# Kernel tuning notes

Measured on AMD Instinct MI355X. Metric: run time of the kernel, lower is better.

The kernel has to match this reference:

```python
import jax, jax.numpy as jnp
import numpy as np

B, S, T, D = 8, 8, 256, 256          # batch, series, time_steps, input_dim
H, DK = 8, 64                         # attn_heads, attn_dim
HD = H * DK                           # 512
L = 2                                 # attn_layers
F = 256                               # mlp_dim
R = 512                               # resolution
M = 128                               # number of mid-points sampled this step
EPS = 1e-5


def setup_inputs() -> dict:
    key = jax.random.key(0)
    ks = iter(jax.random.split(key, 64))

    def rn(shape, scale=0.05):
        return scale * jax.random.normal(next(ks), shape, dtype=jnp.float32)

    inp = {
        'encoded': jax.random.normal(next(ks), (B, S, T, D), dtype=jnp.float32),
        'true_u': jax.random.uniform(next(ks), (B, S, T), dtype=jnp.float32),
        'mid_idx': jnp.sort(jax.random.randint(next(ks), (M,), 0, T)),
        'left_idx': jax.random.randint(next(ks), (M,), 0, T),
        'right_idx': jax.random.randint(next(ks), (M,), 0, T),
        'i': 3,
        # dimension_shift
        'ds_W': rn((D, HD)), 'ds_b': jnp.zeros((HD,), jnp.float32),
        # per-layer, per-head key-creator MLPs (stacked): (D+1) -> F -> F -> DK
        'kW1': rn((L, H, D + 1, F)), 'kb1': jnp.zeros((L, H, F), jnp.float32),
        'kW2': rn((L, H, F, F)),     'kb2': jnp.zeros((L, H, F), jnp.float32),
        'kW3': rn((L, H, F, DK)),    'kb3': jnp.zeros((L, H, DK), jnp.float32),
        # value-creator MLPs
        'vW1': rn((L, H, D + 1, F)), 'vb1': jnp.zeros((L, H, F), jnp.float32),
        'vW2': rn((L, H, F, F)),     'vb2': jnp.zeros((L, H, F), jnp.float32),
        'vW3': rn((L, H, F, DK)),    'vb3': jnp.zeros((L, H, DK), jnp.float32),
        # attention / feed-forward layer norms
        'ln1_g': jnp.ones((L, HD), jnp.float32), 'ln1_b': jnp.zeros((L, HD), jnp.float32),
        'ln2_g': jnp.ones((L, HD), jnp.float32), 'ln2_b': jnp.zeros((L, HD), jnp.float32),
        # feed-forwards
        'ffW1': rn((L, HD, HD)), 'ffb1': jnp.zeros((L, HD), jnp.float32),
        'ffW2': rn((L, HD, HD)), 'ffb2': jnp.zeros((L, HD), jnp.float32),
        # dist_extractors MLP: HD -> F -> F -> R
        'deW1': rn((HD, F)), 'deb1': jnp.zeros((F,), jnp.float32),
        'deW2': rn((F, F)),  'deb2': jnp.zeros((F,), jnp.float32),
        'deW3': rn((F, R)),  'deb3': jnp.zeros((R,), jnp.float32),
    }
    return inp


def _mlp_heads(x, W1, b1, W2, b2, W3, b3):
    # x: [B,S,T,D+1]; weights: [L,H,...] -> out [L,B,S,T,H,DK]
    h = jax.nn.relu(jnp.einsum('bstc,lhcf->lbsthf', x, W1) + b1[:, None, None, None])
    h = jax.nn.relu(jnp.einsum('lbsthf,lhfg->lbsthg', h, W2) + b2[:, None, None, None])
    return jnp.einsum('lbsthg,lhgd->lbsthd', h, W3) + b3[:, None, None, None]


def _ln(x, g, b):
    mu = jnp.mean(x, axis=-1, keepdims=True)
    var = jnp.mean(jnp.square(x - mu), axis=-1, keepdims=True)
    return (x - mu) * jax.lax.rsqrt(var + EPS) * g + b


def reference(encoded, true_u, mid_idx, left_idx, right_idx, i,
              ds_W, ds_b,
              kW1, kb1, kW2, kb2, kW3, kb3,
              vW1, vb1, vW2, vb2, vW3, vb3,
              ln1_g, ln1_b, ln2_g, ln2_b,
              ffW1, ffb1, ffW2, ffb2,
              deW1, deb1, deW2, deb2, deW3, deb3):
    # merged_input = cat([encoded, true_u[..., None]])  -> [B,S,T,D+1]
    merged = jnp.concatenate([encoded, true_u[..., None]], axis=-1)

    keys = _mlp_heads(merged, kW1, kb1, kW2, kb2, kW3, kb3)   # [L,B,S,T,H,DK]
    values = _mlp_heads(merged, vW1, vb1, vW2, vb2, vW3, vb3)  # [L,B,S,T,H,DK]

    srange = jnp.arange(S)
    # n=1 neighbor: time index = loop counter m for series < i, else right[m]
    # (faithful to keys_hist[:, :i, mid:mid+1] in the original)
    idx1 = jnp.where(srange[None, :] < i, jnp.arange(M)[:, None], right_idx[:, None])  # [M,S]

    def gather_neighbors(kv):  # kv: [L,B,S,T,H,DK] -> [L,B,M,S,2,H,DK]
        n0 = jnp.transpose(kv[:, :, :, left_idx], (0, 1, 3, 2, 4, 5))  # [L,B,M,S,H,DK]
        n1 = kv[:, :, srange[None, :], idx1]                            # [L,B,M,S,H,DK]
        return jnp.stack([n0, n1], axis=4)

    nk = gather_neighbors(keys)
    nv = gather_neighbors(values)

    pred = encoded[:, i, mid_idx]                  # [B,M,D]
    att_value = pred @ ds_W + ds_b                 # [B,M,HD]

    scale = DK ** (-0.5)
    for l in range(L):
        avh = att_value.reshape(B, M, H, DK)
        prod = jnp.einsum('bmhd,bmsnhd->bmhsn', avh, nk[l]) * scale
        w = jax.nn.softmax(prod, axis=-1)          # softmax over n only, as in source
        att = jnp.einsum('bmhsn,bmsnhd->bmhd', w, nv[l]).reshape(B, M, HD)
        x = _ln(att_value + att, ln1_g[l], ln1_b[l])
        ff = jax.nn.relu(x @ ffW1[l] + ffb1[l]) @ ffW2[l] + ffb2[l]
        att_value = _ln(x + ff, ln2_g[l], ln2_b[l])

    h = jax.nn.relu(att_value @ deW1 + deb1)
    h = jax.nn.relu(h @ deW2 + deb2)
    logits = h @ deW3 + deb3                       # [B,M,R]
    return logits
```

## Files before the change

### kernel.cpp

```cpp
#include <hip/hip_runtime.h>
#include <hip/hip_bf16.h>

#define NB 8
#define NS 8
#define NT 256
#define ND 256
#define NH 8
#define NDK 64
#define NHD 512
#define NL 2
#define NF 256
#define NR 512
#define NM 128
#define NTOK 16384
#define NROW 1024

typedef __attribute__((ext_vector_type(8))) short short8;
typedef __attribute__((ext_vector_type(4))) float f32x4;

__device__ __forceinline__ unsigned short f2bf(float x) {
    unsigned u = __builtin_bit_cast(unsigned, x);
    unsigned r = (u + 0x7fffu + ((u >> 16) & 1u)) >> 16;
    return (unsigned short)r;
}
__device__ __forceinline__ float bf2f(unsigned short x) {
    return __builtin_bit_cast(float, ((unsigned)x) << 16);
}
__device__ __forceinline__ float wred(float v) {
#pragma unroll
    for (int o = 32; o > 0; o >>= 1) v += __shfl_xor(v, o, 64);
    return v;
}

__device__ __forceinline__ int SW(int row, int scol) {
    return row * 256 + (((scol >> 3) ^ (row & 7)) << 3) + (scol & 7);
}

__global__ __launch_bounds__(256) void prep_all(
    const float* __restrict__ enc,
    const float* __restrict__ kW1, const float* __restrict__ kW2, const float* __restrict__ kW3,
    const float* __restrict__ vW1, const float* __restrict__ vW2, const float* __restrict__ vW3,
    const float* __restrict__ dsW, const float* __restrict__ ffW1,
    const float* __restrict__ ffW2, const float* __restrict__ deW1,
    const float* __restrict__ deW2, const float* __restrict__ deW3,
    unsigned short* __restrict__ XF, unsigned short* __restrict__ WP,
    float* __restrict__ W1L, unsigned short* __restrict__ WG) {
    __shared__ float T[32][257];
    int bid = blockIdx.x, tid = threadIdx.x;
    if (bid < 512) {
        int t0 = bid * 32;
        const float* src = enc + (size_t)t0 * 256;
#pragma unroll
        for (int it = 0; it < 8; ++it) {
            int f4 = it * 256 + tid;
            int row = f4 >> 6, c = (f4 & 63) * 4;
            float4 v = *(const float4*)(src + row * 256 + c);
            T[row][c] = v.x; T[row][c + 1] = v.y; T[row][c + 2] = v.z; T[row][c + 3] = v.w;
        }
        __syncthreads();
        int tile = t0 >> 7, g = (t0 >> 6) & 1, nt0 = (t0 >> 4) & 3;
#pragma unroll
        for (int i = 0; i < 32; i += 8) {
            int o = tid * 32 + i;
            int lane = (o >> 3) & 63, ntp = (o >> 9) & 1, kc = o >> 10;
            int id = lane & 15, quad = lane >> 4;
            __align__(16) unsigned short p[8];
#pragma unroll
            for (int j = 0; j < 8; ++j) p[j] = f2bf(T[ntp * 16 + id][kc * 32 + quad * 8 + j]);
            size_t dsto = ((size_t)((((tile * 8 + kc) * 2 + g) * 4 + (nt0 + ntp)) * 64 + lane)) * 8;
            *(uint4*)(XF + dsto) = *(uint4*)p;
        }
    } else if (bid < 1280) {
        int lb = bid - 512;
        int combo = lb / 24, r = lb % 24;
        int st = r >> 3, kc = r & 7;
        int kvv = combo >> 4, l = (combo >> 3) & 1, h = combo & 7;
        unsigned short* dstc = WP + (size_t)combo * 147456;
        if (st < 2) {
            const float* W = (st == 0) ? (kvv ? vW1 : kW1) : (kvv ? vW2 : kW2);
            int rows = (st == 0) ? 257 : 256;
            const float* src = W + ((size_t)(l * 8 + h) * rows + kc * 32) * 256;
#pragma unroll
            for (int it = 0; it < 8; ++it) {
                int f4 = it * 256 + tid;
                int row = f4 >> 6, c = (f4 & 63) * 4;
                float4 v = *(const float4*)(src + (size_t)row * 256 + c);
                T[row][c] = v.x; T[row][c + 1] = v.y; T[row][c + 2] = v.z; T[row][c + 3] = v.w;
            }
            __syncthreads();
            unsigned short* dst = dstc + st * 65536 + kc * 8192;
#pragma unroll
            for (int i = 0; i < 32; i += 8) {
                int o = tid * 32 + i;
                int lane = (o >> 3) & 63, ftile = o >> 9;
                int id = lane & 15, quad = lane >> 4;
                __align__(16) unsigned short p[8];
#pragma unroll
                for (int j = 0; j < 8; ++j) p[j] = f2bf(T[quad * 8 + j][ftile * 16 + id]);
                *(uint4*)(dst + o) = *(uint4*)p;
            }
            if (st == 0 && kc == 0) {
                const float* hw = (kvv ? vW1 : kW1) + (size_t)(l * 8 + h) * 257 * 256;
                W1L[combo * 256 + tid] = hw[65536 + tid];
            }
        } else {
            const float* src = (kvv ? vW3 : kW3) + ((size_t)(l * 8 + h) * 256 + kc * 32) * 64;
#pragma unroll
            for (int it = 0; it < 2; ++it) {
                int f4 = it * 256 + tid;
                int row = f4 >> 4, c = (f4 & 15) * 4;
                float4 v = *(const float4*)(src + (size_t)row * 64 + c);
                T[row][c] = v.x; T[row][c + 1] = v.y; T[row][c + 2] = v.z; T[row][c + 3] = v.w;
            }
            __syncthreads();
            unsigned short* dst = dstc + 131072 + kc * 2048;
            int o = tid * 8;
            int lane = tid & 63, ftile = tid >> 6;
            int id = lane & 15, quad = lane >> 4;
// ... 145 lines not shown
        for (int j = 0; j < 4; ++j) acc[i][j] = (f32x4){0.f, 0.f, 0.f, 0.f};
#pragma unroll
    for (int kc = 0; kc < 8; ++kc) {
        short8 tn[4];
        LDW(kc + 10, tn);
        short8 bf[4];
#pragma unroll
        for (int nt = 0; nt < 4; ++nt)
            bf[nt] = *(const short8*)(smem + SW(wt * 64 + nt * 16 + id, kc * 32 + quad * 8));
#pragma unroll
        for (int ft = 0; ft < 4; ++ft)
#pragma unroll
            for (int nt = 0; nt < 4; ++nt)
                acc[ft][nt] = __builtin_amdgcn_mfma_f32_16x16x32_bf16(afb[kc & 1][ft], bf[nt], acc[ft][nt], 0, 0, 0);
#pragma unroll
        for (int ft = 0; ft < 4; ++ft) afb[kc & 1][ft] = tn[ft];
    }
    __syncthreads();
#pragma unroll
    for (int ft = 0; ft < 4; ++ft) {
        int fb = wf * 64 + ft * 16 + quad * 4;
        float4 bb = *(const float4*)(b2 + fb);
        const float* bbp = (const float*)&bb;
#pragma unroll
        for (int nt = 0; nt < 4; ++nt) {
            int row = wt * 64 + nt * 16 + id;
            unsigned short p[4];
#pragma unroll
            for (int r = 0; r < 4; ++r)
                p[r] = f2bf(fmaxf(acc[ft][nt][r] + bbp[r], 0.f));
            uint2 pk;
            pk.x = (unsigned)p[0] | ((unsigned)p[1] << 16);
            pk.y = (unsigned)p[2] | ((unsigned)p[3] << 16);
            *(uint2*)(smem + SW(row, fb)) = pk;
        }
    }
    __syncthreads();

    f32x4 a3[4];
#pragma unroll
    for (int i = 0; i < 4; ++i) a3[i] = (f32x4){0.f, 0.f, 0.f, 0.f};
#pragma unroll
    for (int kc = 0; kc < 8; ++kc) {
        short8 tn[4];
        if (kc + 18 < 24) LDW(kc + 18, tn);
        short8 b3f = *(const short8*)(smem + SW(wave * 16 + id, kc * 32 + quad * 8));
#pragma unroll
        for (int ft = 0; ft < 4; ++ft)
            a3[ft] = __builtin_amdgcn_mfma_f32_16x16x32_bf16(afb[kc & 1][ft], b3f, a3[ft], 0, 0, 0);
        if (kc + 18 < 24) {
#pragma unroll
            for (int ft = 0; ft < 4; ++ft) afb[kc & 1][ft] = tn[ft];
        }
    }
    __syncthreads();
    {
        int tl = wave * 16 + id;
#pragma unroll
        for (int ft = 0; ft < 4; ++ft) {
            int dk0 = ft * 16 + quad * 4;
            float4 bb = *(const float4*)(b3 + dk0);
            const float* bbp = (const float*)&bb;
            unsigned short p[4];
#pragma unroll
            for (int r = 0; r < 4; ++r) p[r] = f2bf(a3[ft][r] + bbp[r]);
            uint2 pk;
            pk.x = (unsigned)p[0] | ((unsigned)p[1] << 16);
            pk.y = (unsigned)p[2] | ((unsigned)p[3] << 16);
            *(uint2*)(smem + (size_t)tl * 72 + dk0) = pk;
        }
    }
    __syncthreads();
    {
#pragma unroll
        for (int it = 0; it < 2; ++it) {
            int tl = it * 64 + (tid >> 3), part = tid & 7;
            uint4 v = *(const uint4*)(smem + (size_t)tl * 72 + part * 8);
            size_t base = ((size_t)combo << 20) + (size_t)(r0 + tl) * 64 + part * 8;
            *(uint4*)(KV + base) = v;
        }
    }
}

__global__ __launch_bounds__(256) void gemm_ds(
    const float* __restrict__ enc, const int* __restrict__ mid,
    const int* __restrict__ ip, const unsigned short* __restrict__ WF,
    const float* __restrict__ bias, float* __restrict__ outf) {
    int tid = threadIdx.x, wv = tid >> 6, lane = tid & 63;
    int id = lane & 15, quad = lane >> 4;
    int ntile = blockIdx.x * 4 + wv;
    int n0 = ntile * 16, m0 = blockIdx.y * 16;
    int iv = ip[0];
    int r0 = m0 + id;
    const float* a0p = enc + (((size_t)((r0 >> 7) * 8 + iv)) * 256 + mid[r0 & 127]) * 256 + quad * 8;
    f32x4 acc0 = (f32x4){0.f, 0.f, 0.f, 0.f};
#pragma unroll
    for (int kc = 0; kc < 8; ++kc) {
        short8 bw = *(const short8*)(WF + (size_t)((kc * 32 + ntile) * 64 + lane) * 8);
        float4 u0 = *(const float4*)(a0p + kc * 32);
        float4 u1 = *(const float4*)(a0p + kc * 32 + 4);
        short8 a0;
        a0[0] = (short)f2bf(u0.x); a0[1] = (short)f2bf(u0.y); a0[2] = (short)f2bf(u0.z); a0[3] = (short)f2bf(u0.w);
        a0[4] = (short)f2bf(u1.x); a0[5] = (short)f2bf(u1.y); a0[6] = (short)f2bf(u1.z); a0[7] = (short)f2bf(u1.w);
        acc0 = __builtin_amdgcn_mfma_f32_16x16x32_bf16(a0, bw, acc0, 0, 0, 0);
    }
    float bv = bias[n0 + id];
#pragma unroll
    for (int r = 0; r < 4; ++r) {
        int row = m0 + quad * 4 + r;
        outf[(size_t)row * 512 + n0 + id] = acc0[r] + bv;
    }
}

__global__ __launch_bounds__(512) void layer_fused(
    const unsigned short* __restrict__ KV,
    const int* __restrict__ left, const int* __restrict__ right,
    const int* __restrict__ ip,
    const float* __restrict__ g1, const float* __restrict__ bb1,
    const unsigned short* __restrict__ Wff1, const float* __restrict__ fb1,
    const unsigned short* __restrict__ Wff2, const float* __restrict__ fb2,
    const float* __restrict__ g2, const float* __restrict__ bb2,
    float* __restrict__ ATTV, unsigned short* __restrict__ ATTVB, int l) {
    __shared__ float XF32[16][516];
    __shared__ unsigned short XB16[16][520];
    __shared__ unsigned short F1[16][520];
    const int tid = threadIdx.x, wave = tid >> 6, lane = tid & 63;
    const int id = lane & 15, quad = lane >> 4;
    const int m0 = blockIdx.x * 16;
    const int iv = ip[0];

#pragma unroll
    for (int rr = 0; rr < 2; ++rr) {
        int r = wave * 2 + rr;
        int gid = m0 + r;
        int b = gid >> 7, m = gid & 127;
        int lt = left[m], rt = right[m];
        int h = lane >> 3, d8 = lane & 7;
        const unsigned short* kb = KV + ((size_t)(l * 8 + h) << 20);
        const unsigned short* vb = KV + ((size_t)(16 + l * 8 + h) << 20);
        float av8[8], att8[8];
        {
            const float* avp = ATTV + (size_t)gid * 512 + lane * 8;
            float4 u0 = *(const float4*)(avp);
            float4 u1 = *(const float4*)(avp + 4);
            av8[0] = u0.x; av8[1] = u0.y; av8[2] = u0.z; av8[3] = u0.w;
            av8[4] = u1.x; av8[5] = u1.y; av8[6] = u1.z; av8[7] = u1.w;
        }
#pragma unroll
        for (int j = 0; j < 8; ++j) att8[j] = 0.f;
#pragma unroll 2
        for (int s = 0; s < 8; ++s) {
            int t1 = (s < iv) ? m : rt;
            size_t o0 = (size_t)((b * 8 + s) * 256 + lt) * 64 + d8 * 8;
            size_t o1 = (size_t)((b * 8 + s) * 256 + t1) * 64 + d8 * 8;
            uint4 k0u = *(const uint4*)(kb + o0);
            uint4 k1u = *(const uint4*)(kb + o1);
            uint4 v0u = *(const uint4*)(vb + o0);
            uint4 v1u = *(const uint4*)(vb + o1);
            const unsigned short* k0 = (const unsigned short*)&k0u;
            const unsigned short* k1 = (const unsigned short*)&k1u;
            const unsigned short* v0 = (const unsigned short*)&v0u;
            const unsigned short* v1 = (const unsigned short*)&v1u;
            float p0 = 0.f, p1 = 0.f;
#pragma unroll
            for (int j = 0; j < 8; ++j) {
                p0 += av8[j] * bf2f(k0[j]);
                p1 += av8[j] * bf2f(k1[j]);
            }
#pragma unroll
            for (int o = 1; o < 8; o <<= 1) {
                p0 += __shfl_xor(p0, o, 64);
                p1 += __shfl_xor(p1, o, 64);
            }
            p0 *= 0.125f; p1 *= 0.125f;
            float mx = fmaxf(p0, p1);
            float e0 = __expf(p0 - mx), e1 = __expf(p1 - mx);
            float inv = 1.f / (e0 + e1);
            float w0 = e0 * inv, w1 = e1 * inv;
#pragma unroll
            for (int j = 0; j < 8; ++j)
                att8[j] += w0 * bf2f(v0[j]) + w1 * bf2f(v1[j]);
        }
        float x8[8], sum = 0.f;
#pragma unroll
        for (int j = 0; j < 8; ++j) { x8[j] = av8[j] + att8[j]; sum += x8[j]; }
        float mu = wred(sum) * (1.f / 512.f);
        float s2 = 0.f;
#pragma unroll
        for (int j = 0; j < 8; ++j) { float d = x8[j] - mu; s2 += d * d; }
        float rs = rsqrtf(wred(s2) * (1.f / 512.f) + 1e-5f);
        const float* gp = g1 + lane * 8;
        const float* bp = bb1 + lane * 8;
        __align__(16) float vout[8];
        __align__(16) unsigned short pb[8];
#pragma unroll
        for (int j = 0; j < 8; ++j) {
            float v = (x8[j] - mu) * rs * gp[j] + bp[j];
            vout[j] = v; pb[j] = f2bf(v);
        }
        *(float4*)(&XF32[r][lane * 8]) = *(float4*)vout;
        *(float4*)(&XF32[r][lane * 8 + 4]) = *(float4*)(vout + 4);
        *(uint4*)(&XB16[r][lane * 8]) = *(uint4*)pb;
    }
    __syncthreads();

    {
        f32x4 acc[4];
#pragma unroll
        for (int i = 0; i < 4; ++i) acc[i] = (f32x4){0.f, 0.f, 0.f, 0.f};
        short8 bw[4], a0;
#pragma unroll
        for (int nt = 0; nt < 4; ++nt)
            bw[nt] = *(const short8*)(Wff1 + (size_t)((wave * 4 + nt) * 64 + lane) * 8);
        a0 = *(const short8*)(&XB16[id][quad * 8]);
        for (int kc = 0; kc < 16; ++kc) {
            short8 bwn[4], a0n;
            if (kc + 1 < 16) {
#pragma unroll
                for (int nt = 0; nt < 4; ++nt)
                    bwn[nt] = *(const short8*)(Wff1 + (size_t)(((kc + 1) * 32 + wave * 4 + nt) * 64 + lane) * 8);
                a0n = *(const short8*)(&XB16[id][(kc + 1) * 32 + quad * 8]);
            }
#pragma unroll
            for (int nt = 0; nt < 4; ++nt)
                acc[nt] = __builtin_amdgcn_mfma_f32_16x16x32_bf16(a0, bw[nt], acc[nt], 0, 0, 0);
#pragma unroll
            for (int nt = 0; nt < 4; ++nt) bw[nt] = bwn[nt];
            a0 = a0n;
        }
#pragma unroll
        for (int nt = 0; nt < 4; ++nt) {
            int n0 = (wave * 4 + nt) * 16;
            float bv = fb1[n0 + id];
#pragma unroll
            for (int r = 0; r < 4; ++r)
                F1[quad * 4 + r][n0 + id] = f2bf(fmaxf(acc[nt][r] + bv, 0.f));
        }
    }
    __syncthreads();

    {
        f32x4 acc[4];
#pragma unroll
        for (int i = 0; i < 4; ++i) acc[i] = (f32x4){0.f, 0.f, 0.f, 0.f};
        short8 bw[4], a0;
#pragma unroll
        for (int nt = 0; nt < 4; ++nt)
            bw[nt] = *(const short8*)(Wff2 + (size_t)((wave * 4 + nt) * 64 + lane) * 8);
        a0 = *(const short8*)(&F1[id][quad * 8]);
        for (int kc = 0; kc < 16; ++kc) {
            short8 bwn[4], a0n;
            if (kc + 1 < 16) {
#pragma unroll
                for (int nt = 0; nt < 4; ++nt)
                    bwn[nt] = *(const short8*)(Wff2 + (size_t)(((kc + 1) * 32 + wave * 4 + nt) * 64 + lane) * 8);
                a0n = *(const short8*)(&F1[id][(kc + 1) * 32 + quad * 8]);
            }
#pragma unroll
            for (int nt = 0; nt < 4; ++nt)
                acc[nt] = __builtin_amdgcn_mfma_f32_16x16x32_bf16(a0, bw[nt], acc[nt], 0, 0, 0);
#pragma unroll
            for (int nt = 0; nt < 4; ++nt) bw[nt] = bwn[nt];
            a0 = a0n;
        }
#pragma unroll
        for (int nt = 0; nt < 4; ++nt) {
            int n0 = (wave * 4 + nt) * 16;
            float bv = fb2[n0 + id];
#pragma unroll
            for (int r = 0; r < 4; ++r)
                XF32[quad * 4 + r][n0 + id] += acc[nt][r] + bv;
        }
    }
    __syncthreads();

#pragma unroll
    for (int rr = 0; rr < 2; ++rr) {
        int r = wave * 2 + rr;
        int gid = m0 + r;
        float x8[8];
        {
            float4 u0 = *(const float4*)(&XF32[r][lane * 8]);
            float4 u1 = *(const float4*)(&XF32[r][lane * 8 + 4]);
            x8[0] = u0.x; x8[1] = u0.y; x8[2] = u0.z; x8[3] = u0.w;
            x8[4] = u1.x; x8[5] = u1.y; x8[6] = u1.z; x8[7] = u1.w;
        }
        float sum = 0.f;
#pragma unroll
        for (int j = 0; j < 8; ++j) sum += x8[j];
        float mu = wred(sum) * (1.f / 512.f);
        float s2 = 0.f;
#pragma unroll
        for (int j = 0; j < 8; ++j) { float d = x8[j] - mu; s2 += d * d; }
        float rs = rsqrtf(wred(s2) * (1.f / 512.f) + 1e-5f);
        const float* gp = g2 + lane * 8;
        const float* bp = bb2 + lane * 8;
        float* of = ATTV + (size_t)gid * 512 + lane * 8;
        unsigned short* ob = ATTVB + (size_t)gid * 512 + lane * 8;
        __align__(16) float vout[8];
        __align__(16) unsigned short pb[8];
#pragma unroll
        for (int j = 0; j < 8; ++j) {
            float v = (x8[j] - mu) * rs * gp[j] + bp[j];
            vout[j] = v; pb[j] = f2bf(v);
        }
        *(float4*)(of) = *(float4*)vout;
        *(float4*)(of + 4) = *(float4*)(vout + 4);
        *(uint4*)(ob) = *(uint4*)pb;
    }
}

__global__ __launch_bounds__(512) void decoder_fused(
    const unsigned short* __restrict__ A,
    const unsigned short* __restrict__ W1, const float* __restrict__ bv1,
    const unsigned short* __restrict__ W2, const float* __restrict__ bv2,
    const unsigned short* __restrict__ W3, const float* __restrict__ bv3,
    float* __restrict__ out) {
    __shared__ unsigned short D1[16][264];
    __shared__ unsigned short D2[16][264];
    const int tid = threadIdx.x, wave = tid >> 6, lane = tid & 63;
    const int id = lane & 15, quad = lane >> 4;
    const int m0 = blockIdx.x * 16;

    {
        f32x4 acc[2];
        acc[0] = (f32x4){0.f, 0.f, 0.f, 0.f};
        acc[1] = (f32x4){0.f, 0.f, 0.f, 0.f};
        short8 bw[2], a0;
#pragma unroll
        for (int nt = 0; nt < 2; ++nt)
            bw[nt] = *(const short8*)(W1 + (size_t)((wave * 2 + nt) * 64 + lane) * 8);
        a0 = *(const short8*)(A + (size_t)(m0 + id) * 512 + quad * 8);
        for (int kc = 0; kc < 16; ++kc) {
            short8 bwn[2], a0n;
            if (kc + 1 < 16) {
#pragma unroll
                for (int nt = 0; nt < 2; ++nt)
                    bwn[nt] = *(const short8*)(W1 + (size_t)(((kc + 1) * 16 + wave * 2 + nt) * 64 + lane) * 8);
                a0n = *(const short8*)(A + (size_t)(m0 + id) * 512 + (kc + 1) * 32 + quad * 8);
            }
#pragma unroll
            for (int nt = 0; nt < 2; ++nt)
                acc[nt] = __builtin_amdgcn_mfma_f32_16x16x32_bf16(a0, bw[nt], acc[nt], 0, 0, 0);
#pragma unroll
            for (int nt = 0; nt < 2; ++nt) bw[nt] = bwn[nt];
            a0 = a0n;
        }
#pragma unroll
        for (int nt = 0; nt < 2; ++nt) {
            int n0 = (wave * 2 + nt) * 16;
            float bv = bv1[n0 + id];
#pragma unroll
            for (int r = 0; r < 4; ++r)
                D1[quad * 4 + r][n0 + id] = f2bf(fmaxf(acc[nt][r] + bv, 0.f));
        }
    }
    __syncthreads();

    {
        f32x4 acc[2];
        acc[0] = (f32x4){0.f, 0.f, 0.f, 0.f};
        acc[1] = (f32x4){0.f, 0.f, 0.f, 0.f};
        for (int kc = 0; kc < 8; ++kc) {
            short8 a0 = *(const short8*)(&D1[id][kc * 32 + quad * 8]);
#pragma unroll
            for (int nt = 0; nt < 2; ++nt) {
                short8 bw = *(const short8*)(W2 + (size_t)((kc * 16 + wave * 2 + nt) * 64 + lane) * 8);
                acc[nt] = __builtin_amdgcn_mfma_f32_16x16x32_bf16(a0, bw, acc[nt], 0, 0, 0);
            }
        }
#pragma unroll
        for (int nt = 0; nt < 2; ++nt) {
            int n0 = (wave * 2 + nt) * 16;
            float bv = bv2[n0 + id];
#pragma unroll
            for (int r = 0; r < 4; ++r)
                D2[quad * 4 + r][n0 + id] = f2bf(fmaxf(acc[nt][r] + bv, 0.f));
        }
    }
    __syncthreads();

    {
        f32x4 acc[4];
#pragma unroll
        for (int i = 0; i < 4; ++i) acc[i] = (f32x4){0.f, 0.f, 0.f, 0.f};
        for (int kc = 0; kc < 8; ++kc) {
            short8 a0 = *(const short8*)(&D2[id][kc * 32 + quad * 8]);
#pragma unroll
            for (int nt = 0; nt < 4; ++nt) {
                short8 bw = *(const short8*)(W3 + (size_t)((kc * 32 + wave * 4 + nt) * 64 + lane) * 8);
                acc[nt] = __builtin_amdgcn_mfma_f32_16x16x32_bf16(a0, bw, acc[nt], 0, 0, 0);
            }
        }
#pragma unroll
        for (int nt = 0; nt < 4; ++nt) {
            int n0 = (wave * 4 + nt) * 16;
            float bv = bv3[n0 + id];
#pragma unroll
            for (int r = 0; r < 4; ++r)
                out[(size_t)(m0 + quad * 4 + r) * 512 + n0 + id] = acc[nt][r] + bv;
        }
    }
}

extern "C" void kernel_launch(void* const* d_in, const int* in_sizes, int n_in,
                              void* d_out, int out_size, void* d_ws, size_t ws_size,
                              hipStream_t stream) {
    const float* encoded = (const float*)d_in[0];
    const float* true_u  = (const float*)d_in[1];
    const int* mid_idx   = (const int*)d_in[2];
    const int* left_idx  = (const int*)d_in[3];
    const int* right_idx = (const int*)d_in[4];
    const int* ip        = (const int*)d_in[5];
    const float* ds_W = (const float*)d_in[6];
    const float* ds_b = (const float*)d_in[7];
    const float* kW1 = (const float*)d_in[8];
    const float* kb1 = (const float*)d_in[9];
    const float* kW2 = (const float*)d_in[10];
    const float* kb2 = (const float*)d_in[11];
    const float* kW3 = (const float*)d_in[12];
    const float* kb3 = (const float*)d_in[13];
    const float* vW1 = (const float*)d_in[14];
    const float* vb1 = (const float*)d_in[15];
    const float* vW2 = (const float*)d_in[16];
    const float* vb2 = (const float*)d_in[17];
    const float* vW3 = (const float*)d_in[18];
    const float* vb3 = (const float*)d_in[19];
    const float* ln1_g = (const float*)d_in[20];
    const float* ln1_b = (const float*)d_in[21];
    const float* ln2_g = (const float*)d_in[22];
    const float* ln2_b = (const float*)d_in[23];
    const float* ffW1 = (const float*)d_in[24];
    const float* ffb1 = (const float*)d_in[25];
    const float* ffW2 = (const float*)d_in[26];
    const float* ffb2 = (const float*)d_in[27];
    const float* deW1 = (const float*)d_in[28];
    const float* deb1 = (const float*)d_in[29];
    const float* deW2 = (const float*)d_in[30];
    const float* deb2 = (const float*)d_in[31];
    const float* deW3 = (const float*)d_in[32];
    const float* deb3 = (const float*)d_in[33];

    char* ws = (char*)d_ws;
    unsigned short* XF    = (unsigned short*)(ws + 0);
    unsigned short* WP    = (unsigned short*)(ws + 8388608);
    float* W1L            = (float*)(ws + 17825792);
    unsigned short* KV    = (unsigned short*)(ws + 17858560);
    unsigned short* WG    = (unsigned short*)(ws + 84967424);
    float* ATTV           = (float*)(ws + 87982080);
    unsigned short* ATTVB = (unsigned short*)(ws + 94273536);

    unsigned short* WGds    = WG + 0;
    unsigned short* WGff1_0 = WG + 131072;
    unsigned short* WGff1_1 = WG + 393216;
    unsigned short* WGff2_0 = WG + 655360;
    unsigned short* WGff2_1 = WG + 917504;
    unsigned short* WGde1   = WG + 1179648;
    unsigned short* WGde2   = WG + 1310720;
    unsigned short* WGde3   = WG + 1376256;

    prep_all<<<1648, 256, 0, stream>>>(encoded, kW1, kW2, kW3, vW1, vW2, vW3,
                                       ds_W, ffW1, ffW2, deW1, deW2, deW3,
                                       XF, WP, W1L, WG);
    heads_mlp<<<4096, 512, 0, stream>>>(true_u, XF, WP, W1L, kb1, kb2, kb3,
                                        vb1, vb2, vb3, KV);
    gemm_ds<<<dim3(8, 64), 256, 0, stream>>>(encoded, mid_idx, ip, WGds, ds_b, ATTV);
    for (int l = 0; l < 2; ++l) {
        layer_fused<<<64, 512, 0, stream>>>(KV, left_idx, right_idx, ip,
                                            ln1_g + l * 512, ln1_b + l * 512,
                                            (l ? WGff1_1 : WGff1_0), ffb1 + l * 512,
                                            (l ? WGff2_1 : WGff2_0), ffb2 + l * 512,
                                            ln2_g + l * 512, ln2_b + l * 512,
                                            ATTV, ATTVB, l);
    }
    decoder_fused<<<64, 512, 0, stream>>>(ATTVB, WGde1, deb1, WGde2, deb2,
                                          WGde3, deb3, (float*)d_out);
}
```

Baseline: 377.1 us.

## Fuse ds projection, both attention layers and decoder into one tail kernel

```diff
diff --git a/kernel.cpp b/kernel.cpp
--- a/kernel.cpp
+++ b/kernel.cpp
@@ -34,6 +34,9 @@
 
 __device__ __forceinline__ int SW(int row, int scol) {
     return row * 256 + (((scol >> 3) ^ (row & 7)) << 3) + (scol & 7);
+}
+__device__ __forceinline__ int SW32(int row, int col) {
+    return row * 512 + (((col >> 2) ^ (row & 7)) << 2) + (col & 3);
 }
 
 __global__ __launch_bounds__(256) void prep_all(
@@ -345,245 +348,253 @@
     }
 }
 
-__global__ __launch_bounds__(256) void gemm_ds(
+__global__ __launch_bounds__(512) void tail_fused(
     const float* __restrict__ enc, const int* __restrict__ mid,
-    const int* __restrict__ ip, const unsigned short* __restrict__ WF,
-    const float* __restrict__ bias, float* __restrict__ outf) {
-    int tid = threadIdx.x, wv = tid >> 6, lane = tid & 63;
-    int id = lane & 15, quad = lane >> 4;
-    int ntile = blockIdx.x * 4 + wv;
-    int n0 = ntile * 16, m0 = blockIdx.y * 16;
-    int iv = ip[0];
-    int r0 = m0 + id;
-    const float* a0p = enc + (((size_t)((r0 >> 7) * 8 + iv)) * 256 + mid[r0 & 127]) * 256 + quad * 8;
-    f32x4 acc0 = (f32x4){0.f, 0.f, 0.f, 0.f};
-#pragma unroll
-    for (int kc = 0; kc < 8; ++kc) {
-        short8 bw = *(const short8*)(WF + (size_t)((kc * 32 + ntile) * 64 + lane) * 8);
-        float4 u0 = *(const float4*)(a0p + kc * 32);
-        float4 u1 = *(const float4*)(a0p + kc * 32 + 4);
-        short8 a0;
-        a0[0] = (short)f2bf(u0.x); a0[1] = (short)f2bf(u0.y); a0[2] = (short)f2bf(u0.z); a0[3] = (short)f2bf(u0.w);
-        a0[4] = (short)f2bf(u1.x); a0[5] = (short)f2bf(u1.y); a0[6] = (short)f2bf(u1.z); a0[7] = (short)f2bf(u1.w);
-        acc0 = __builtin_amdgcn_mfma_f32_16x16x32_bf16(a0, bw, acc0, 0, 0, 0);
-    }
-    float bv = bias[n0 + id];
-#pragma unroll
-    for (int r = 0; r < 4; ++r) {
-        int row = m0 + quad * 4 + r;
-        outf[(size_t)row * 512 + n0 + id] = acc0[r] + bv;
-    }
-}
-
-__global__ __launch_bounds__(512) void layer_fused(
+    const int* __restrict__ ip,
+    const unsigned short* __restrict__ WGds, const float* __restrict__ dsb,
     const unsigned short* __restrict__ KV,
     const int* __restrict__ left, const int* __restrict__ right,
-    const int* __restrict__ ip,
-    const float* __restrict__ g1, const float* __restrict__ bb1,
-    const unsigned short* __restrict__ Wff1, const float* __restrict__ fb1,
-    const unsigned short* __restrict__ Wff2, const float* __restrict__ fb2,
-    const float* __restrict__ g2, const float* __restrict__ bb2,
-    float* __restrict__ ATTV, unsigned short* __restrict__ ATTVB, int l) {
-    __shared__ float XF32[16][516];
-    __shared__ unsigned short XB16[16][520];
-    __shared__ unsigned short F1[16][520];
+    const float* __restrict__ ln1_g, const float* __restrict__ ln1_b,
+    const float* __restrict__ ln2_g, const float* __restrict__ ln2_b,
+    const unsigned short* __restrict__ Wff1_0, const unsigned short* __restrict__ Wff1_1,
+    const float* __restrict__ ffb1,
+    const unsigned short* __restrict__ Wff2_0, const unsigned short* __restrict__ Wff2_1,
+    const float* __restrict__ ffb2,
+    const unsigned short* __restrict__ Wde1, const float* __restrict__ deb1,
+    const unsigned short* __restrict__ Wde2, const float* __restrict__ deb2,
+    const unsigned short* __restrict__ Wde3, const float* __restrict__ deb3,
+    float* __restrict__ out) {
+    __shared__ __align__(16) char SMEM[65536];
+    float* AV = (float*)SMEM;
+    float* XW = (float*)(SMEM + 32768);
+    unsigned short* F1 = (unsigned short*)SMEM;
+    unsigned short* XD = (unsigned short*)SMEM;
+    unsigned short* D1 = (unsigned short*)(SMEM + 32768);
+    unsigned short* D2 = (unsigned short*)(SMEM + 32768 + 8448);
+
     const int tid = threadIdx.x, wave = tid >> 6, lane = tid & 63;
     const int id = lane & 15, quad = lane >> 4;
     const int m0 = blockIdx.x * 16;
     const int iv = ip[0];
 
-#pragma unroll
-    for (int rr = 0; rr < 2; ++rr) {
-        int r = wave * 2 + rr;
-        int gid = m0 + r;
-        int b = gid >> 7, m = gid & 127;
-        int lt = left[m], rt = right[m];
-        int h = lane >> 3, d8 = lane & 7;
-        const unsigned short* kb = KV + ((size_t)(l * 8 + h) << 20);
-        const unsigned short* vb = KV + ((size_t)(16 + l * 8 + h) << 20);
-        float av8[8], att8[8];
-        {
-            const float* avp = ATTV + (size_t)gid * 512 + lane * 8;
-            float4 u0 = *(const float4*)(avp);
-            float4 u1 = *(const float4*)(avp + 4);
-            av8[0] = u0.x; av8[1] = u0.y; av8[2] = u0.z; av8[3] = u0.w;
-            av8[4] = u1.x; av8[5] = u1.y; av8[6] = u1.z; av8[7] = u1.w;
-        }
-#pragma unroll
-        for (int j = 0; j < 8; ++j) att8[j] = 0.f;
-#pragma unroll 2
-        for (int s = 0; s < 8; ++s) {
-            int t1 = (s < iv) ? m : rt;
-            size_t o0 = (size_t)((b * 8 + s) * 256 + lt) * 64 + d8 * 8;
-            size_t o1 = (size_t)((b * 8 + s) * 256 + t1) * 64 + d8 * 8;
-            uint4 k0u = *(const uint4*)(kb + o0);
-            uint4 k1u = *(const uint4*)(kb + o1);
-            uint4 v0u = *(const uint4*)(vb + o0);
-            uint4 v1u = *(const uint4*)(vb + o1);
-            const unsigned short* k0 = (const unsigned short*)&k0u;
-            const unsigned short* k1 = (const unsigned short*)&k1u;
-            const unsigned short* v0 = (const unsigned short*)&v0u;
-            const unsigned short* v1 = (const unsigned short*)&v1u;
-            float p0 = 0.f, p1 = 0.f;
-#pragma unroll
-            for (int j = 0; j < 8; ++j) {
-                p0 += av8[j] * bf2f(k0[j]);
-                p1 += av8[j] * bf2f(k1[j]);
-            }
-#pragma unroll
-            for (int o = 1; o < 8; o <<= 1) {
-                p0 += __shfl_xor(p0, o, 64);
-                p1 += __shfl_xor(p1, o, 64);
-            }
-            p0 *= 0.125f; p1 *= 0.125f;
-            float mx = fmaxf(p0, p1);
-            float e0 = __expf(p0 - mx), e1 = __expf(p1 - mx);
-            float inv = 1.f / (e0 + e1);
-            float w0 = e0 * inv, w1 = e1 * inv;
-#pragma unroll
-            for (int j = 0; j < 8; ++j)
-                att8[j] += w0 * bf2f(v0[j]) + w1 * bf2f(v1[j]);
-        }
-        float x8[8], sum = 0.f;
-#pragma unroll
-        for (int j = 0; j < 8; ++j) { x8[j] = av8[j] + att8[j]; sum += x8[j]; }
-        float mu = wred(sum) * (1.f / 512.f);
-        float s2 = 0.f;
-#pragma unroll
-        for (int j = 0; j < 8; ++j) { float d = x8[j] - mu; s2 += d * d; }
-        float rs = rsqrtf(wred(s2) * (1.f / 512.f) + 1e-5f);
-        const float* gp = g1 + lane * 8;
-        const float* bp = bb1 + lane * 8;
-        __align__(16) float vout[8];
-        __align__(16) unsigned short pb[8];
-#pragma unroll
-        for (int j = 0; j < 8; ++j) {
-            float v = (x8[j] - mu) * rs * gp[j] + bp[j];
-            vout[j] = v; pb[j] = f2bf(v);
-        }
-        *(float4*)(&XF32[r][lane * 8]) = *(float4*)vout;
-        *(float4*)(&XF32[r][lane * 8 + 4]) = *(float4*)(vout + 4);
-        *(uint4*)(&XB16[r][lane * 8]) = *(uint4*)pb;
-    }
-    __syncthreads();
-
     {
+        int r0g = m0 + id;
+        const float* a0p = enc + (((size_t)((r0g >> 7) * 8 + iv)) * 256 + mid[r0g & 127]) * 256 + quad * 8;
         f32x4 acc[4];
 #pragma unroll
         for (int i = 0; i < 4; ++i) acc[i] = (f32x4){0.f, 0.f, 0.f, 0.f};
-        short8 bw[4], a0;
-#pragma unroll
-        for (int nt = 0; nt < 4; ++nt)
-            bw[nt] = *(const short8*)(Wff1 + (size_t)((wave * 4 + nt) * 64 + lane) * 8);
-        a0 = *(const short8*)(&XB16[id][quad * 8]);
-        for (int kc = 0; kc < 16; ++kc) {
-            short8 bwn[4], a0n;
-            if (kc + 1 < 16) {
-#pragma unroll
-                for (int nt = 0; nt < 4; ++nt)
-                    bwn[nt] = *(const short8*)(Wff1 + (size_t)(((kc + 1) * 32 + wave * 4 + nt) * 64 + lane) * 8);
-                a0n = *(const short8*)(&XB16[id][(kc + 1) * 32 + quad * 8]);
-            }
-#pragma unroll
-            for (int nt = 0; nt < 4; ++nt)
-                acc[nt] = __builtin_amdgcn_mfma_f32_16x16x32_bf16(a0, bw[nt], acc[nt], 0, 0, 0);
-#pragma unroll
-            for (int nt = 0; nt < 4; ++nt) bw[nt] = bwn[nt];
-            a0 = a0n;
+#pragma unroll
+        for (int kc = 0; kc < 8; ++kc) {
+            float4 u0 = *(const float4*)(a0p + kc * 32);
+            float4 u1 = *(const float4*)(a0p + kc * 32 + 4);
+            short8 a0;
+            a0[0] = (short)f2bf(u0.x); a0[1] = (short)f2bf(u0.y); a0[2] = (short)f2bf(u0.z); a0[3] = (short)f2bf(u0.w);
+            a0[4] = (short)f2bf(u1.x); a0[5] = (short)f2bf(u1.y); a0[6] = (short)f2bf(u1.z); a0[7] = (short)f2bf(u1.w);
+#pragma unroll
+            for (int nt = 0; nt < 4; ++nt) {
+                int ntile = wave * 4 + nt;
+                short8 bw = *(const short8*)(WGds + (size_t)((kc * 32 + ntile) * 64 + lane) * 8);
+                acc[nt] = __builtin_amdgcn_mfma_f32_16x16x32_bf16(a0, bw, acc[nt], 0, 0, 0);
+            }
         }
 #pragma unroll
         for (int nt = 0; nt < 4; ++nt) {
             int n0 = (wave * 4 + nt) * 16;
-            float bv = fb1[n0 + id];
+            float bv = dsb[n0 + id];
 #pragma unroll
             for (int r = 0; r < 4; ++r)
-                F1[quad * 4 + r][n0 + id] = f2bf(fmaxf(acc[nt][r] + bv, 0.f));
-        }
-    }
-    __syncthreads();
-
-    {
-        f32x4 acc[4];
-#pragma unroll
-        for (int i = 0; i < 4; ++i) acc[i] = (f32x4){0.f, 0.f, 0.f, 0.f};
-        short8 bw[4], a0;
-#pragma unroll
-        for (int nt = 0; nt < 4; ++nt)
-            bw[nt] = *(const short8*)(Wff2 + (size_t)((wave * 4 + nt) * 64 + lane) * 8);
-        a0 = *(const short8*)(&F1[id][quad * 8]);
-        for (int kc = 0; kc < 16; ++kc) {
-            short8 bwn[4], a0n;
-            if (kc + 1 < 16) {
+                AV[SW32(quad * 4 + r, n0 + id)] = acc[nt][r] + bv;
+        }
+    }
+    __syncthreads();
+
+    for (int l = 0; l < 2; ++l) {
+        const float* g1 = ln1_g + l * 512;
+        const float* bb1 = ln1_b + l * 512;
+        const float* g2 = ln2_g + l * 512;
+        const float* bb2 = ln2_b + l * 512;
+        const unsigned short* Wf1 = l ? Wff1_1 : Wff1_0;
+        const unsigned short* Wf2 = l ? Wff2_1 : Wff2_0;
+        const float* fb1 = ffb1 + l * 512;
+        const float* fb2 = ffb2 + l * 512;
+
+#pragma unroll
+        for (int rr = 0; rr < 2; ++rr) {
+            int r = wave * 2 + rr;
+            int gid = m0 + r;
+            int b = gid >> 7, m = gid & 127;
+            int lt = left[m], rt = right[m];
+            int h = lane >> 3, d8 = lane & 7;
+            const unsigned short* kb = KV + ((size_t)(l * 8 + h) << 20);
+            const unsigned short* vb = KV + ((size_t)(16 + l * 8 + h) << 20);
+            float av8[8], att8[8];
+            {
+                float4 u0 = *(const float4*)(&AV[SW32(r, lane * 8)]);
+                float4 u1 = *(const float4*)(&AV[SW32(r, lane * 8 + 4)]);
+                av8[0] = u0.x; av8[1] = u0.y; av8[2] = u0.z; av8[3] = u0.w;
+                av8[4] = u1.x; av8[5] = u1.y; av8[6] = u1.z; av8[7] = u1.w;
+            }
+#pragma unroll
+            for (int j = 0; j < 8; ++j) att8[j] = 0.f;
+#pragma unroll 2
+            for (int s = 0; s < 8; ++s) {
+                int t1 = (s < iv) ? m : rt;
+                size_t o0 = (size_t)((b * 8 + s) * 256 + lt) * 64 + d8 * 8;
+                size_t o1 = (size_t)((b * 8 + s) * 256 + t1) * 64 + d8 * 8;
+                uint4 k0u = *(const uint4*)(kb + o0);
+                uint4 k1u = *(const uint4*)(kb + o1);
+                uint4 v0u = *(const uint4*)(vb + o0);
+                uint4 v1u = *(const uint4*)(vb + o1);
+                const unsigned short* k0 = (const unsigned short*)&k0u;
+                const unsigned short* k1 = (const unsigned short*)&k1u;
+                const unsigned short* v0 = (const unsigned short*)&v0u;
+                const unsigned short* v1 = (const unsigned short*)&v1u;
+                float p0 = 0.f, p1 = 0.f;
+#pragma unroll
+                for (int j = 0; j < 8; ++j) {
+                    p0 += av8[j] * bf2f(k0[j]);
+                    p1 += av8[j] * bf2f(k1[j]);
+                }
+#pragma unroll
+                for (int o = 1; o < 8; o <<= 1) {
+                    p0 += __shfl_xor(p0, o, 64);
+                    p1 += __shfl_xor(p1, o, 64);
+                }
+                p0 *= 0.125f; p1 *= 0.125f;
+                float mx = fmaxf(p0, p1);
+                float e0 = __expf(p0 - mx), e1 = __expf(p1 - mx);
+                float inv = 1.f / (e0 + e1);
+                float w0 = e0 * inv, w1 = e1 * inv;
+#pragma unroll
+                for (int j = 0; j < 8; ++j)
+                    att8[j] += w0 * bf2f(v0[j]) + w1 * bf2f(v1[j]);
+            }
+            float x8[8], sum = 0.f;
+#pragma unroll
+            for (int j = 0; j < 8; ++j) { x8[j] = av8[j] + att8[j]; sum += x8[j]; }
+            float mu = wred(sum) * (1.f / 512.f);
+            float s2 = 0.f;
+#pragma unroll
+            for (int j = 0; j < 8; ++j) { float d = x8[j] - mu; s2 += d * d; }
+            float rs = rsqrtf(wred(s2) * (1.f / 512.f) + 1e-5f);
+            const float* gp = g1 + lane * 8;
+            const float* bp = bb1 + lane * 8;
+            __align__(16) float vout[8];
+#pragma unroll
+            for (int j = 0; j < 8; ++j) vout[j] = (x8[j] - mu) * rs * gp[j] + bp[j];
+            *(float4*)(&XW[SW32(r, lane * 8)]) = *(float4*)vout;
+            *(float4*)(&XW[SW32(r, lane * 8 + 4)]) = *(float4*)(vout + 4);
+        }
+        __syncthreads();
+
+        {
+            f32x4 acc[4];
+#pragma unroll
+            for (int i = 0; i < 4; ++i) acc[i] = (f32x4){0.f, 0.f, 0.f, 0.f};
+            short8 bw[4];
+#pragma unroll
+            for (int nt = 0; nt < 4; ++nt)
+                bw[nt] = *(const short8*)(Wf1 + (size_t)((wave * 4 + nt) * 64 + lane) * 8);
+            for (int kc = 0; kc < 16; ++kc) {
+                short8 bwn[4];
+                if (kc + 1 < 16) {
+#pragma unroll
+                    for (int nt = 0; nt < 4; ++nt)
+                        bwn[nt] = *(const short8*)(Wf1 + (size_t)(((kc + 1) * 32 + wave * 4 + nt) * 64 + lane) * 8);
+                }
+                float4 u0 = *(const float4*)(&XW[SW32(id, kc * 32 + quad * 8)]);
+                float4 u1 = *(const float4*)(&XW[SW32(id, kc * 32 + quad * 8 + 4)]);
+                short8 a0;
+                a0[0] = (short)f2bf(u0.x); a0[1] = (short)f2bf(u0.y); a0[2] = (short)f2bf(u0.z); a0[3] = (short)f2bf(u0.w);
+                a0[4] = (short)f2bf(u1.x); a0[5] = (short)f2bf(u1.y); a0[6] = (short)f2bf(u1.z); a0[7] = (short)f2bf(u1.w);
 #pragma unroll
                 for (int nt = 0; nt < 4; ++nt)
-                    bwn[nt] = *(const short8*)(Wff2 + (size_t)(((kc + 1) * 32 + wave * 4 + nt) * 64 + lane) * 8);
-                a0n = *(const short8*)(&F1[id][(kc + 1) * 32 + quad * 8]);
-            }
+                    acc[nt] = __builtin_amdgcn_mfma_f32_16x16x32_bf16(a0, bw[nt], acc[nt], 0, 0, 0);
+#pragma unroll
+                for (int nt = 0; nt < 4; ++nt) bw[nt] = bwn[nt];
+            }
+            __syncthreads();
+#pragma unroll
+            for (int nt = 0; nt < 4; ++nt) {
+                int n0 = (wave * 4 + nt) * 16;
+                float bv = fb1[n0 + id];
+#pragma unroll
+                for (int r = 0; r < 4; ++r)
+                    F1[(quad * 4 + r) * 520 + n0 + id] = f2bf(fmaxf(acc[nt][r] + bv, 0.f));
+            }
+        }
+        __syncthreads();
+
+        {
+            f32x4 acc[4];
+#pragma unroll
+            for (int i = 0; i < 4; ++i) acc[i] = (f32x4){0.f, 0.f, 0.f, 0.f};
+            short8 bw[4], a0;
 #pragma unroll
             for (int nt = 0; nt < 4; ++nt)
-                acc[nt] = __builtin_amdgcn_mfma_f32_16x16x32_bf16(a0, bw[nt], acc[nt], 0, 0, 0);
-#pragma unroll
-            for (int nt = 0; nt < 4; ++nt) bw[nt] = bwn[nt];
-            a0 = a0n;
-        }
-#pragma unroll
-        for (int nt = 0; nt < 4; ++nt) {
-            int n0 = (wave * 4 + nt) * 16;
-            float bv = fb2[n0 + id];
-#pragma unroll
-            for (int r = 0; r < 4; ++r)
-                XF32[quad * 4 + r][n0 + id] += acc[nt][r] + bv;
-        }
-    }
-    __syncthreads();
-
-#pragma unroll
-    for (int rr = 0; rr < 2; ++rr) {
-        int r = wave * 2 + rr;
-        int gid = m0 + r;
-        float x8[8];
-        {
-            float4 u0 = *(const float4*)(&XF32[r][lane * 8]);
-            float4 u1 = *(const float4*)(&XF32[r][lane * 8 + 4]);
-            x8[0] = u0.x; x8[1] = u0.y; x8[2] = u0.z; x8[3] = u0.w;
-            x8[4] = u1.x; x8[5] = u1.y; x8[6] = u1.z; x8[7] = u1.w;
-        }
-        float sum = 0.f;
-#pragma unroll
-        for (int j = 0; j < 8; ++j) sum += x8[j];
-        float mu = wred(sum) * (1.f / 512.f);
-        float s2 = 0.f;
-#pragma unroll
-        for (int j = 0; j < 8; ++j) { float d = x8[j] - mu; s2 += d * d; }
-        float rs = rsqrtf(wred(s2) * (1.f / 512.f) + 1e-5f);
-        const float* gp = g2 + lane * 8;
-        const float* bp = bb2 + lane * 8;
-        float* of = ATTV + (size_t)gid * 512 + lane * 8;
-        unsigned short* ob = ATTVB + (size_t)gid * 512 + lane * 8;
-        __align__(16) float vout[8];
-        __align__(16) unsigned short pb[8];
-#pragma unroll
-        for (int j = 0; j < 8; ++j) {
-            float v = (x8[j] - mu) * rs * gp[j] + bp[j];
-            vout[j] = v; pb[j] = f2bf(v);
-        }
-        *(float4*)(of) = *(float4*)vout;
-        *(float4*)(of + 4) = *(float4*)(vout + 4);
-        *(uint4*)(ob) = *(uint4*)pb;
-    }
-}
-
-__global__ __launch_bounds__(512) void decoder_fused(
-    const unsigned short* __restrict__ A,
-    const unsigned short* __restrict__ W1, const float* __restrict__ bv1,
-    const unsigned short* __restrict__ W2, const float* __restrict__ bv2,
-    const unsigned short* __restrict__ W3, const float* __restrict__ bv3,
-    float* __restrict__ out) {
-    __shared__ unsigned short D1[16][264];
-    __shared__ unsigned short D2[16][264];
-    const int tid = threadIdx.x, wave = tid >> 6, lane = tid & 63;
-    const int id = lane & 15, quad = lane >> 4;
-    const int m0 = blockIdx.x * 16;
+                bw[nt] = *(const short8*)(Wf2 + (size_t)((wave * 4 + nt) * 64 + lane) * 8);
+            a0 = *(const short8*)(&F1[id * 520 + quad * 8]);
+            for (int kc = 0; kc < 16; ++kc) {
+                short8 bwn[4], a0n;
+                if (kc + 1 < 16) {
+#pragma unroll
+                    for (int nt = 0; nt < 4; ++nt)
+                        bwn[nt] = *(const short8*)(Wf2 + (size_t)(((kc + 1) * 32 + wave * 4 + nt) * 64 + lane) * 8);
+                    a0n = *(const short8*)(&F1[id * 520 + (kc + 1) * 32 + quad * 8]);
+                }
+#pragma unroll
+                for (int nt = 0; nt < 4; ++nt)
+                    acc[nt] = __builtin_amdgcn_mfma_f32_16x16x32_bf16(a0, bw[nt], acc[nt], 0, 0, 0);
+#pragma unroll
+                for (int nt = 0; nt < 4; ++nt) bw[nt] = bwn[nt];
+                a0 = a0n;
+            }
+#pragma unroll
+            for (int nt = 0; nt < 4; ++nt) {
+                int n0 = (wave * 4 + nt) * 16;
+                float bv = fb2[n0 + id];
+#pragma unroll
+                for (int r = 0; r < 4; ++r)
+                    XW[SW32(quad * 4 + r, n0 + id)] += acc[nt][r] + bv;
+            }
+        }
+        __syncthreads();
+
+#pragma unroll
+        for (int rr = 0; rr < 2; ++rr) {
+            int r = wave * 2 + rr;
+            float x8[8];
+            {
+                float4 u0 = *(const float4*)(&XW[SW32(r, lane * 8)]);
+                float4 u1 = *(const float4*)(&XW[SW32(r, lane * 8 + 4)]);
+                x8[0] = u0.x; x8[1] = u0.y; x8[2] = u0.z; x8[3] = u0.w;
+                x8[4] = u1.x; x8[5] = u1.y; x8[6] = u1.z; x8[7] = u1.w;
+            }
+            float sum = 0.f;
+#pragma unroll
+            for (int j = 0; j < 8; ++j) sum += x8[j];
+            float mu = wred(sum) * (1.f / 512.f);
+            float s2 = 0.f;
+#pragma unroll
+            for (int j = 0; j < 8; ++j) { float d = x8[j] - mu; s2 += d * d; }
+            float rs = rsqrtf(wred(s2) * (1.f / 512.f) + 1e-5f);
+            const float* gp = g2 + lane * 8;
+            const float* bp = bb2 + lane * 8;
+            __align__(16) float vout[8];
+#pragma unroll
+            for (int j = 0; j < 8; ++j) vout[j] = (x8[j] - mu) * rs * gp[j] + bp[j];
+            if (l == 0) {
+                *(float4*)(&AV[SW32(r, lane * 8)]) = *(float4*)vout;
+                *(float4*)(&AV[SW32(r, lane * 8 + 4)]) = *(float4*)(vout + 4);
+            } else {
+                __align__(16) unsigned short pb[8];
+#pragma unroll
+                for (int j = 0; j < 8; ++j) pb[j] = f2bf(vout[j]);
+                *(uint4*)(&XD[r * 520 + lane * 8]) = *(uint4*)pb;
+            }
+        }
+        __syncthreads();
+    }
 
     {
         f32x4 acc[2];
@@ -592,15 +603,15 @@
         short8 bw[2], a0;
 #pragma unroll
         for (int nt = 0; nt < 2; ++nt)
-            bw[nt] = *(const short8*)(W1 + (size_t)((wave * 2 + nt) * 64 + lane) * 8);
-        a0 = *(const short8*)(A + (size_t)(m0 + id) * 512 + quad * 8);
+            bw[nt] = *(const short8*)(Wde1 + (size_t)((wave * 2 + nt) * 64 + lane) * 8);
+        a0 = *(const short8*)(&XD[id * 520 + quad * 8]);
         for (int kc = 0; kc < 16; ++kc) {
             short8 bwn[2], a0n;
             if (kc + 1 < 16) {
 #pragma unroll
                 for (int nt = 0; nt < 2; ++nt)
-                    bwn[nt] = *(const short8*)(W1 + (size_t)(((kc + 1) * 16 + wave * 2 + nt) * 64 + lane) * 8);
-                a0n = *(const short8*)(A + (size_t)(m0 + id) * 512 + (kc + 1) * 32 + quad * 8);
+                    bwn[nt] = *(const short8*)(Wde1 + (size_t)(((kc + 1) * 16 + wave * 2 + nt) * 64 + lane) * 8);
+                a0n = *(const short8*)(&XD[id * 520 + (kc + 1) * 32 + quad * 8]);
             }
 #pragma unroll
             for (int nt = 0; nt < 2; ++nt)
@@ -609,56 +620,55 @@
             for (int nt = 0; nt < 2; ++nt) bw[nt] = bwn[nt];
             a0 = a0n;
         }
+        __syncthreads();
 #pragma unroll
         for (int nt = 0; nt < 2; ++nt) {
             int n0 = (wave * 2 + nt) * 16;
-            float bv = bv1[n0 + id];
+            float bv = deb1[n0 + id];
 #pragma unroll
             for (int r = 0; r < 4; ++r)
-                D1[quad * 4 + r][n0 + id] = f2bf(fmaxf(acc[nt][r] + bv, 0.f));
-        }
-    }
-    __syncthreads();
-
+                D1[(quad * 4 + r) * 264 + n0 + id] = f2bf(fmaxf(acc[nt][r] + bv, 0.f));
+        }
+    }
+    __syncthreads();
     {
         f32x4 acc[2];
         acc[0] = (f32x4){0.f, 0.f, 0.f, 0.f};
         acc[1] = (f32x4){0.f, 0.f, 0.f, 0.f};
         for (int kc = 0; kc < 8; ++kc) {
-            short8 a0 = *(const short8*)(&D1[id][kc * 32 + quad * 8]);
+            short8 a0 = *(const short8*)(&D1[id * 264 + kc * 32 + quad * 8]);
 #pragma unroll
             for (int nt = 0; nt < 2; ++nt) {
-                short8 bw = *(const short8*)(W2 + (size_t)((kc * 16 + wave * 2 + nt) * 64 + lane) * 8);
+                short8 bw = *(const short8*)(Wde2 + (size_t)((kc * 16 + wave * 2 + nt) * 64 + lane) * 8);
                 acc[nt] = __builtin_amdgcn_mfma_f32_16x16x32_bf16(a0, bw, acc[nt], 0, 0, 0);
             }
         }
 #pragma unroll
         for (int nt = 0; nt < 2; ++nt) {
             int n0 = (wave * 2 + nt) * 16;
-            float bv = bv2[n0 + id];
+            float bv = deb2[n0 + id];
 #pragma unroll
             for (int r = 0; r < 4; ++r)
-                D2[quad * 4 + r][n0 + id] = f2bf(fmaxf(acc[nt][r] + bv, 0.f));
-        }
-    }
-    __syncthreads();
-
+                D2[(quad * 4 + r) * 264 + n0 + id] = f2bf(fmaxf(acc[nt][r] + bv, 0.f));
+        }
+    }
+    __syncthreads();
     {
         f32x4 acc[4];
 #pragma unroll
         for (int i = 0; i < 4; ++i) acc[i] = (f32x4){0.f, 0.f, 0.f, 0.f};
         for (int kc = 0; kc < 8; ++kc) {
-            short8 a0 = *(const short8*)(&D2[id][kc * 32 + quad * 8]);
+            short8 a0 = *(const short8*)(&D2[id * 264 + kc * 32 + quad * 8]);
 #pragma unroll
             for (int nt = 0; nt < 4; ++nt) {
-                short8 bw = *(const short8*)(W3 + (size_t)((kc * 32 + wave * 4 + nt) * 64 + lane) * 8);
+                short8 bw = *(const short8*)(Wde3 + (size_t)((kc * 32 + wave * 4 + nt) * 64 + lane) * 8);
                 acc[nt] = __builtin_amdgcn_mfma_f32_16x16x32_bf16(a0, bw, acc[nt], 0, 0, 0);
             }
         }
 #pragma unroll
         for (int nt = 0; nt < 4; ++nt) {
             int n0 = (wave * 4 + nt) * 16;
-            float bv = bv3[n0 + id];
+            float bv = deb3[n0 + id];
 #pragma unroll
             for (int r = 0; r < 4; ++r)
                 out[(size_t)(m0 + quad * 4 + r) * 512 + n0 + id] = acc[nt][r] + bv;
@@ -710,8 +720,6 @@
     float* W1L            = (float*)(ws + 17825792);
     unsigned short* KV    = (unsigned short*)(ws + 17858560);
     unsigned short* WG    = (unsigned short*)(ws + 84967424);
-    float* ATTV           = (float*)(ws + 87982080);
-    unsigned short* ATTVB = (unsigned short*)(ws + 94273536);
 
     unsigned short* WGds    = WG + 0;
     unsigned short* WGff1_0 = WG + 131072;
@@ -727,15 +735,11 @@
                                        XF, WP, W1L, WG);
     heads_mlp<<<4096, 512, 0, stream>>>(true_u, XF, WP, W1L, kb1, kb2, kb3,
                                         vb1, vb2, vb3, KV);
-    gemm_ds<<<dim3(8, 64), 256, 0, stream>>>(encoded, mid_idx, ip, WGds, ds_b, ATTV);
-    for (int l = 0; l < 2; ++l) {
-        layer_fused<<<64, 512, 0, stream>>>(KV, left_idx, right_idx, ip,
-                                            ln1_g + l * 512, ln1_b + l * 512,
-                                            (l ? WGff1_1 : WGff1_0), ffb1 + l * 512,
-                                            (l ? WGff2_1 : WGff2_0), ffb2 + l * 512,
-                                            ln2_g + l * 512, ln2_b + l * 512,
-                                            ATTV, ATTVB, l);
-    }
-    decoder_fused<<<64, 512, 0, stream>>>(ATTVB, WGde1, deb1, WGde2, deb2,
-                                          WGde3, deb3, (float*)d_out);
-}
+    tail_fused<<<64, 512, 0, stream>>>(encoded, mid_idx, ip, WGds, ds_b, KV,
+                                       left_idx, right_idx,
+                                       ln1_g, ln1_b, ln2_g, ln2_b,
+                                       WGff1_0, WGff1_1, ffb1,
+                                       WGff2_0, WGff2_1, ffb2,
+                                       WGde1, deb1, WGde2, deb2, WGde3, deb3,
+                                       (float*)d_out);
+}
```

Result: faster. 368.9 us, median of 2 (-2.2%).
